# Kernel optimization log

Measured on AMD Instinct MI355X. Metric: run time of the kernel, lower is better.

## Reference

```python
import jax, jax.numpy as jnp
import numpy as np

N = 50000      # nodes
E = 1_600_000  # edges
FN = 8         # num_node_features
FE = 8         # num_edge_features
H = 16         # hidden_layers[0]
IH = 10        # intra_hidden


def _lin(k, i, o):
    return (jax.random.normal(k, (i, o), dtype=jnp.float32) / np.sqrt(i)).astype(jnp.float32)


def setup_inputs() -> dict:
    key = jax.random.key(0)
    ks = jax.random.split(key, 16)
    d = {}
    d["x"] = jax.random.normal(ks[0], (N, FN), dtype=jnp.float32)
    d["edge_attr"] = jax.random.normal(ks[1], (E, FE), dtype=jnp.float32)
    d["edge_index"] = jax.random.randint(ks[2], (2, E), 0, N)
    # NNConv 0: in=FN, out=H; edge-nn: FE -> IH -> FN*H
    d["c0_w1"] = _lin(ks[3], FE, IH);  d["c0_b1"] = jnp.zeros((IH,), jnp.float32)
    d["c0_w2"] = _lin(ks[4], IH, FN * H); d["c0_b2"] = jnp.zeros((FN * H,), jnp.float32)
    d["c0_root"] = _lin(ks[5], FN, H); d["c0_bias"] = jnp.zeros((H,), jnp.float32)
    # NNConv 1: in=H, out=IH; edge-nn: FE -> IH -> H*IH
    d["c1_w1"] = _lin(ks[6], FE, IH);  d["c1_b1"] = jnp.zeros((IH,), jnp.float32)
    d["c1_w2"] = _lin(ks[7], IH, H * IH); d["c1_b2"] = jnp.zeros((H * IH,), jnp.float32)
    d["c1_root"] = _lin(ks[8], H, IH); d["c1_bias"] = jnp.zeros((IH,), jnp.float32)
    # edge predictor: (FE+IH) -> IH -> 1
    d["ep_w1"] = _lin(ks[9], FE + IH, IH); d["ep_b1"] = jnp.zeros((IH,), jnp.float32)
    d["ep_w2"] = _lin(ks[10], IH, 1); d["ep_b2"] = jnp.zeros((1,), jnp.float32)
    return d


def _nnconv(x, edge_index, edge_attr, w1, b1, w2, b2, root, bias, in_ch, out_ch):
    """PyG NNConv (aggr='add', root_weight=True): per-edge weight from edge MLP,
    gather source features, per-edge matvec, scatter-add to targets, plus root term."""
    src, dst = edge_index[0], edge_index[1]
    w = jax.nn.relu(edge_attr @ w1 + b1) @ w2 + b2        # [E, in*out]
    w = w.reshape(-1, in_ch, out_ch)                       # [E, in, out]
    msg = jnp.einsum('ei,eio->eo', x[src], w)              # [E, out]
    agg = jax.ops.segment_sum(msg, dst, num_segments=x.shape[0])  # [N, out]
    return agg + x @ root + bias


def reference(x, edge_attr, edge_index,
              c0_w1, c0_b1, c0_w2, c0_b2, c0_root, c0_bias,
              c1_w1, c1_b1, c1_w2, c1_b2, c1_root, c1_bias,
              ep_w1, ep_b1, ep_w2, ep_b2):
    h = jax.nn.relu(_nnconv(x, edge_index, edge_attr,
                            c0_w1, c0_b1, c0_w2, c0_b2, c0_root, c0_bias, FN, H))
    h = jax.nn.relu(_nnconv(h, edge_index, edge_attr,
                            c1_w1, c1_b1, c1_w2, c1_b2, c1_root, c1_bias, H, IH))
    feat = jnp.concatenate([edge_attr, h[edge_index[0]]], axis=1)  # [E, FE+IH]
    scores = jax.nn.relu(feat @ ep_w1 + ep_b1) @ ep_w2 + ep_b2     # [E, 1]
    return scores.squeeze(-1)
```

## Files before the change

### kernel.cpp

```cpp
#include <hip/hip_runtime.h>

#define N_NODES 50000
#define E_EDGES 1600000
#define FN 8
#define FE 8
#define HID 16
#define IH 10
#define NB_SCAN 196

#define I_CNT   0
#define I_OFF   50048
#define I_RANK  100096
#define I_BSUM  1700096
#define I_BBASE 1700352
#define I_TOTAL 1700608
#define F_H     0
#define F_H2    800000
#define F_MSG   1300000
#define F_TOTAL 26900000
#define WS_NEED ((size_t)I_TOTAL*4 + (size_t)F_TOTAL*4)

__global__ __launch_bounds__(256) void count_rank_k(
    const int* __restrict__ ei, int* __restrict__ cnt, int* __restrict__ rank)
{
    int e = blockIdx.x * 256 + threadIdx.x;
    if (e >= E_EDGES) return;
    int dst = ei[E_EDGES + e];
    rank[e] = atomicAdd(&cnt[dst], 1);
}

__global__ __launch_bounds__(256) void blocksum_k(
    const int* __restrict__ cnt, int* __restrict__ bsum)
{
    __shared__ int sh[256];
    int t = threadIdx.x;
    int idx = blockIdx.x * 256 + t;
    sh[t] = (idx < N_NODES) ? cnt[idx] : 0;
    __syncthreads();
#pragma unroll
    for (int d = 128; d > 0; d >>= 1) {
        if (t < d) sh[t] += sh[t + d];
        __syncthreads();
    }
    if (t == 0) bsum[blockIdx.x] = sh[0];
}

__global__ __launch_bounds__(256) void scan_bsums_k(
    const int* __restrict__ bsum, int* __restrict__ bbase)
{
    __shared__ int sh[256];
    int t = threadIdx.x;
    int v = (t < NB_SCAN) ? bsum[t] : 0;
    sh[t] = v;
    __syncthreads();
#pragma unroll
    for (int d = 1; d < 256; d <<= 1) {
        int u = (t >= d) ? sh[t - d] : 0;
        __syncthreads();
        sh[t] += u;
        __syncthreads();
    }
    if (t < NB_SCAN) bbase[t] = sh[t] - v;
}

__global__ __launch_bounds__(256) void offsets_k(
    const int* __restrict__ cnt, const int* __restrict__ bbase,
    int* __restrict__ offset)
{
    __shared__ int sh[256];
    int t = threadIdx.x;
    int b = blockIdx.x;
    int idx = b * 256 + t;
    int v = (idx < N_NODES) ? cnt[idx] : 0;
    sh[t] = v;
    __syncthreads();
#pragma unroll
    for (int d = 1; d < 256; d <<= 1) {
        int u = (t >= d) ? sh[t - d] : 0;
        __syncthreads();
        sh[t] += u;
        __syncthreads();
    }
    int incl = sh[t];
    int base = bbase[b];
    if (idx < N_NODES) offset[idx] = base + incl - v;
    if (idx == N_NODES - 1) offset[N_NODES] = base + incl;
}

__device__ __forceinline__ void load8(const float* __restrict__ p, float v[8]) {
    const float4* q = reinterpret_cast<const float4*>(p);
    float4 a = q[0], b = q[1];
    v[0]=a.x; v[1]=a.y; v[2]=a.z; v[3]=a.w;
    v[4]=b.x; v[5]=b.y; v[6]=b.z; v[7]=b.w;
}

__device__ __forceinline__ void edge_mlp_seq(
    const float eav[FE], const float* __restrict__ w1,
    const float* __restrict__ b1, float u[IH])
{
#pragma unroll
    for (int h = 0; h < IH; ++h) u[h] = b1[h];
#pragma unroll
    for (int k = 0; k < FE; ++k) {
        float ek = eav[k];
#pragma unroll
        for (int h = 0; h < IH; ++h) u[h] = fmaf(ek, w1[k*IH + h], u[h]);
    }
#pragma unroll
    for (int h = 0; h < IH; ++h) u[h] = fmaxf(u[h], 0.f);
}

__global__ __launch_bounds__(256) void conv0_scatter_k(
    const float* __restrict__ x, const float* __restrict__ ea,
    const int* __restrict__ ei,
    const float* __restrict__ w1, const float* __restrict__ b1,
    const float* __restrict__ w2, const float* __restrict__ b2,
    const int* __restrict__ offset, const int* __restrict__ rank,
    float* __restrict__ msgbuf)
{
    int e = blockIdx.x * 256 + threadIdx.x;
    if (e >= E_EDGES) return;
    int src = ei[e];
    int dst = ei[E_EDGES + e];

    float eav[FE];
    load8(ea + (size_t)e * FE, eav);
    float u[IH];
    edge_mlp_seq(eav, w1, b1, u);
    float xv[FN];
    load8(x + (size_t)src * FN, xv);

    float msg[HID];
#pragma unroll
    for (int o = 0; o < HID; ++o) msg[o] = 0.f;
#pragma unroll
    for (int i = 0; i < FN; ++i) {
        float xi = xv[i];
#pragma unroll
        for (int o = 0; o < HID; ++o)
            msg[o] = fmaf(xi, b2[i*HID + o], msg[o]);
    }
#pragma unroll
    for (int h = 0; h < IH; ++h) {
        float t[HID];
#pragma unroll
        for (int o = 0; o < HID; ++o) t[o] = 0.f;
        const float* wp = w2 + h * (FN*HID);
#pragma unroll
        for (int i = 0; i < FN; ++i) {
            float xi = xv[i];
#pragma unroll
            for (int o = 0; o < HID; ++o)
                t[o] = fmaf(xi, wp[i*HID + o], t[o]);
        }
        float uh = u[h];
#pragma unroll
        for (int o = 0; o < HID; ++o) msg[o] = fmaf(uh, t[o], msg[o]);
    }

    size_t pos = (size_t)(offset[dst] + rank[e]) * HID;
    float4* mp = reinterpret_cast<float4*>(msgbuf + pos);
    mp[0] = make_float4(msg[0],  msg[1],  msg[2],  msg[3]);
    mp[1] = make_float4(msg[4],  msg[5],  msg[6],  msg[7]);
    mp[2] = make_float4(msg[8],  msg[9],  msg[10], msg[11]);
    mp[3] = make_float4(msg[12], msg[13], msg[14], msg[15]);
}

__global__ __launch_bounds__(256) void node0_red_k(
    const float* __restrict__ x, const float* __restrict__ msgbuf,
    const int* __restrict__ offset,
    const float* __restrict__ root, const float* __restrict__ bias,
    float* __restrict__ h)
{
    int idx = blockIdx.x * 256 + threadIdx.x;
    if (idx >= N_NODES * HID) return;
    int n = idx >> 4;
    int o = idx & 15;
    int beg = offset[n], end = offset[n + 1];
    float s = bias[o];
    for (int j = beg; j < end; ++j) s += msgbuf[(size_t)j * HID + o];
    const float* xr = x + (size_t)n * FN;
#pragma unroll
    for (int i = 0; i < FN; ++i) s = fmaf(xr[i], root[i*HID + o], s);
    h[idx] = fmaxf(s, 0.f);
}

__global__ __launch_bounds__(256) void conv1_scatter_k(
    const float* __restrict__ hin, const float* __restrict__ ea,
    const int* __restrict__ ei,
    const float* __restrict__ w1, const float* __restrict__ b1,
    const float* __restrict__ w2, const float* __restrict__ b2,
    const int* __restrict__ offset, const int* __restrict__ rank,
    float* __restrict__ msgbuf)
{
    int e = blockIdx.x * 256 + threadIdx.x;
    if (e >= E_EDGES) return;
    int src = ei[e];
    int dst = ei[E_EDGES + e];

    float eav[FE];
    load8(ea + (size_t)e * FE, eav);
    float u[IH];
    edge_mlp_seq(eav, w1, b1, u);
    float hv[HID];
    load8(hin + (size_t)src * HID,     hv);
    load8(hin + (size_t)src * HID + 8, hv + 8);

    float msg[IH];
#pragma unroll
    for (int o = 0; o < IH; ++o) msg[o] = 0.f;
#pragma unroll
    for (int i = 0; i < HID; ++i) {
        float hi = hv[i];
#pragma unroll
        for (int o = 0; o < IH; ++o)
            msg[o] = fmaf(hi, b2[i*IH + o], msg[o]);
    }
#pragma unroll
    for (int hh = 0; hh < IH; ++hh) {
        float t[IH];
#pragma unroll
        for (int o = 0; o < IH; ++o) t[o] = 0.f;
        const float* wp = w2 + hh * (HID*IH);
#pragma unroll
        for (int i = 0; i < HID; ++i) {
            float hi = hv[i];
#pragma unroll
            for (int o = 0; o < IH; ++o)
                t[o] = fmaf(hi, wp[i*IH + o], t[o]);
        }
        float uh = u[hh];
#pragma unroll
        for (int o = 0; o < IH; ++o) msg[o] = fmaf(uh, t[o], msg[o]);
    }

    size_t pos = (size_t)(offset[dst] + rank[e]) * IH;
    float2* mp = reinterpret_cast<float2*>(msgbuf + pos);
    mp[0] = make_float2(msg[0], msg[1]);
    mp[1] = make_float2(msg[2], msg[3]);
    mp[2] = make_float2(msg[4], msg[5]);
    mp[3] = make_float2(msg[6], msg[7]);
    mp[4] = make_float2(msg[8], msg[9]);
}

__global__ __launch_bounds__(256) void node1_red_k(
    const float* __restrict__ hin, const float* __restrict__ msgbuf,
    const int* __restrict__ offset,
    const float* __restrict__ root, const float* __restrict__ bias,
    float* __restrict__ h2)
{
    int idx = blockIdx.x * 256 + threadIdx.x;
    if (idx >= N_NODES * IH) return;
    int n = idx / IH;
    int o = idx - n * IH;
    int beg = offset[n], end = offset[n + 1];
    float s = bias[o];
    for (int j = beg; j < end; ++j) s += msgbuf[(size_t)j * IH + o];
    const float* hr = hin + (size_t)n * HID;
#pragma unroll
    for (int i = 0; i < HID; ++i) s = fmaf(hr[i], root[i*IH + o], s);
    h2[idx] = fmaxf(s, 0.f);
}

__global__ __launch_bounds__(256) void edge_pred_k(
    const float* __restrict__ h2, const float* __restrict__ ea,
    const int* __restrict__ ei,
    const float* __restrict__ w1, const float* __restrict__ b1,
    const float* __restrict__ w2, const float* __restrict__ b2,
    float* __restrict__ out)
{
    int e = blockIdx.x * 256 + threadIdx.x;
    if (e >= E_EDGES) return;
    int src = ei[e];
    float eav[FE];
    load8(ea + (size_t)e * FE, eav);
    float hv[IH];
    {
        const float2* p = reinterpret_cast<const float2*>(h2 + (size_t)src * IH);
        float2 a = p[0], b = p[1], c = p[2], d = p[3], f = p[4];
        hv[0]=a.x; hv[1]=a.y; hv[2]=b.x; hv[3]=b.y; hv[4]=c.x;
        hv[5]=c.y; hv[6]=d.x; hv[7]=d.y; hv[8]=f.x; hv[9]=f.y;
    }
    float t[IH];
#pragma unroll
    for (int j = 0; j < IH; ++j) t[j] = b1[j];
#pragma unroll
    for (int k = 0; k < FE; ++k) {
        float ek = eav[k];
#pragma unroll
        for (int j = 0; j < IH; ++j) t[j] = fmaf(ek, w1[k*IH + j], t[j]);
    }
#pragma unroll
    for (int k = 0; k < IH; ++k) {
        float hk = hv[k];
#pragma unroll
        for (int j = 0; j < IH; ++j) t[j] = fmaf(hk, w1[(FE + k)*IH + j], t[j]);
    }
    float score = b2[0];
#pragma unroll
    for (int j = 0; j < IH; ++j)
        score = fmaf(fmaxf(t[j], 0.f), w2[j], score);
    out[e] = score;
}

__global__ __launch_bounds__(256) void conv0_edge_k(
    const float* __restrict__ x, const float* __restrict__ ea,
    const int* __restrict__ ei,
    const float* __restrict__ w1, const float* __restrict__ b1,
    const float* __restrict__ w2, const float* __restrict__ b2,
    float* __restrict__ agg)
{
    int e = blockIdx.x * 256 + threadIdx.x;
    if (e >= E_EDGES) return;
    int src = ei[e];
    int dst = ei[E_EDGES + e];
    float eav[FE];
    load8(ea + (size_t)e * FE, eav);
    float u[IH];
    edge_mlp_seq(eav, w1, b1, u);
    float xv[FN];
    load8(x + (size_t)src * FN, xv);
    float msg[HID];
#pragma unroll
    for (int o = 0; o < HID; ++o) msg[o] = 0.f;
#pragma unroll
    for (int i = 0; i < FN; ++i) {
        float xi = xv[i];
#pragma unroll
        for (int o = 0; o < HID; ++o)
            msg[o] = fmaf(xi, b2[i*HID + o], msg[o]);
    }
#pragma unroll
    for (int h = 0; h < IH; ++h) {
        float t[HID];
#pragma unroll
        for (int o = 0; o < HID; ++o) t[o] = 0.f;
        const float* wp = w2 + h * (FN*HID);
#pragma unroll
        for (int i = 0; i < FN; ++i) {
            float xi = xv[i];
#pragma unroll
            for (int o = 0; o < HID; ++o)
                t[o] = fmaf(xi, wp[i*HID + o], t[o]);
        }
        float uh = u[h];
#pragma unroll
        for (int o = 0; o < HID; ++o) msg[o] = fmaf(uh, t[o], msg[o]);
    }
    float* ap = agg + (size_t)dst * HID;
#pragma unroll
    for (int o = 0; o < HID; ++o) atomicAdd(ap + o, msg[o]);
}

__global__ __launch_bounds__(256) void node0_k(
    const float* __restrict__ x, const float* __restrict__ agg,
    const float* __restrict__ root, const float* __restrict__ bias,
    float* __restrict__ h)
{
    int idx = blockIdx.x * 256 + threadIdx.x;
    if (idx >= N_NODES * HID) return;
    int n = idx >> 4;
    int o = idx & 15;
    float s = agg[idx] + bias[o];
    const float* xr = x + (size_t)n * FN;
#pragma unroll
    for (int i = 0; i < FN; ++i) s = fmaf(xr[i], root[i*HID + o], s);
    h[idx] = fmaxf(s, 0.f);
}

__global__ __launch_bounds__(256) void conv1_edge_k(
    const float* __restrict__ hin, const float* __restrict__ ea,
    const int* __restrict__ ei,
    const float* __restrict__ w1, const float* __restrict__ b1,
    const float* __restrict__ w2, const float* __restrict__ b2,
    float* __restrict__ agg)
{
    int e = blockIdx.x * 256 + threadIdx.x;
    if (e >= E_EDGES) return;
    int src = ei[e];
    int dst = ei[E_EDGES + e];
    float eav[FE];
    load8(ea + (size_t)e * FE, eav);
    float u[IH];
    edge_mlp_seq(eav, w1, b1, u);
    float hv[HID];
    load8(hin + (size_t)src * HID,     hv);
    load8(hin + (size_t)src * HID + 8, hv + 8);
    float msg[IH];
#pragma unroll
    for (int o = 0; o < IH; ++o) msg[o] = 0.f;
#pragma unroll
    for (int i = 0; i < HID; ++i) {
        float hi = hv[i];
#pragma unroll
        for (int o = 0; o < IH; ++o)
            msg[o] = fmaf(hi, b2[i*IH + o], msg[o]);
    }
#pragma unroll
    for (int hh = 0; hh < IH; ++hh) {
        float t[IH];
#pragma unroll
        for (int o = 0; o < IH; ++o) t[o] = 0.f;
        const float* wp = w2 + hh * (HID*IH);
#pragma unroll
        for (int i = 0; i < HID; ++i) {
            float hi = hv[i];
#pragma unroll
            for (int o = 0; o < IH; ++o)
                t[o] = fmaf(hi, wp[i*IH + o], t[o]);
        }
        float uh = u[hh];
#pragma unroll
        for (int o = 0; o < IH; ++o) msg[o] = fmaf(uh, t[o], msg[o]);
    }
    float* ap = agg + (size_t)dst * IH;
#pragma unroll
    for (int o = 0; o < IH; ++o) atomicAdd(ap + o, msg[o]);
}

__global__ __launch_bounds__(256) void node1_k(
    const float* __restrict__ hin, const float* __restrict__ agg,
    const float* __restrict__ root, const float* __restrict__ bias,
    float* __restrict__ h2)
{
    int idx = blockIdx.x * 256 + threadIdx.x;
    if (idx >= N_NODES * IH) return;
    int n = idx / IH;
    int o = idx - n * IH;
    float s = agg[idx] + bias[o];
    const float* hr = hin + (size_t)n * HID;
#pragma unroll
    for (int i = 0; i < HID; ++i) s = fmaf(hr[i], root[i*IH + o], s);
    h2[idx] = fmaxf(s, 0.f);
}

extern "C" void kernel_launch(void* const* d_in, const int* in_sizes, int n_in,
                              void* d_out, int out_size, void* d_ws, size_t ws_size,
                              hipStream_t stream) {
    const float* x       = (const float*)d_in[0];
    const float* ea      = (const float*)d_in[1];
    const int*   ei      = (const int*)  d_in[2];
    const float* c0_w1   = (const float*)d_in[3];
    const float* c0_b1   = (const float*)d_in[4];
    const float* c0_w2   = (const float*)d_in[5];
    const float* c0_b2   = (const float*)d_in[6];
    const float* c0_root = (const float*)d_in[7];
    const float* c0_bias = (const float*)d_in[8];
    const float* c1_w1   = (const float*)d_in[9];
    const float* c1_b1   = (const float*)d_in[10];
    const float* c1_w2   = (const float*)d_in[11];
    const float* c1_b2   = (const float*)d_in[12];
    const float* c1_root = (const float*)d_in[13];
    const float* c1_bias = (const float*)d_in[14];
    const float* ep_w1   = (const float*)d_in[15];
    const float* ep_b1   = (const float*)d_in[16];
    const float* ep_w2   = (const float*)d_in[17];
    const float* ep_b2   = (const float*)d_in[18];
    float* out = (float*)d_out;

    int eb = (E_EDGES + 255) / 256;

    if (ws_size >= WS_NEED) {
        int*   wi     = (int*)d_ws;
        int*   cnt    = wi + I_CNT;
        int*   offset = wi + I_OFF;
        int*   rank   = wi + I_RANK;
        int*   bsum   = wi + I_BSUM;
        int*   bbase  = wi + I_BBASE;
        float* wf     = (float*)(wi + I_TOTAL);
        float* h      = wf + F_H;
        float* h2     = wf + F_H2;
        float* msg    = wf + F_MSG;

        hipMemsetAsync(cnt, 0, N_NODES * sizeof(int), stream);
        count_rank_k<<<eb, 256, 0, stream>>>(ei, cnt, rank);
        blocksum_k<<<NB_SCAN, 256, 0, stream>>>(cnt, bsum);
        scan_bsums_k<<<1, 256, 0, stream>>>(bsum, bbase);
        offsets_k<<<NB_SCAN, 256, 0, stream>>>(cnt, bbase, offset);

        conv0_scatter_k<<<eb, 256, 0, stream>>>(x, ea, ei, c0_w1, c0_b1, c0_w2, c0_b2,
                                                offset, rank, msg);
        node0_red_k<<<(N_NODES*HID + 255)/256, 256, 0, stream>>>(x, msg, offset,
                                                                 c0_root, c0_bias, h);
        conv1_scatter_k<<<eb, 256, 0, stream>>>(h, ea, ei, c1_w1, c1_b1, c1_w2, c1_b2,
                                                offset, rank, msg);
        node1_red_k<<<(N_NODES*IH + 255)/256, 256, 0, stream>>>(h, msg, offset,
                                                                c1_root, c1_bias, h2);
        edge_pred_k<<<eb, 256, 0, stream>>>(h2, ea, ei, ep_w1, ep_b1, ep_w2, ep_b2, out);
    } else {
        float* ws   = (float*)d_ws;
        float* agg0 = ws;
        float* agg1 = ws + 800000;
        float* h    = ws + 1300000;
        float* h2   = ws + 2100000;
        hipMemsetAsync(d_ws, 0, 1300000 * sizeof(float), stream);
        conv0_edge_k<<<eb, 256, 0, stream>>>(x, ea, ei, c0_w1, c0_b1, c0_w2, c0_b2, agg0);
        node0_k<<<(N_NODES*HID + 255)/256, 256, 0, stream>>>(x, agg0, c0_root, c0_bias, h);
        conv1_edge_k<<<eb, 256, 0, stream>>>(h, ea, ei, c1_w1, c1_b1, c1_w2, c1_b2, agg1);
        node1_k<<<(N_NODES*IH + 255)/256, 256, 0, stream>>>(h, agg1, c1_root, c1_bias, h2);
        edge_pred_k<<<eb, 256, 0, stream>>>(h2, ea, ei, ep_w1, ep_b1, ep_w2, ep_b2, out);
    }
}
```

Baseline: 300.1 us.

## Write edge messages in edge order and gather via CSR permutation in reduction

Instead of scattering each edge message to its destination-sorted slot using rank, the conv kernels now write messages contiguously by edge index. A separate cursor and perm pass builds a destination-sorted edge permutation, and the node reduction kernels read messages indirectly through it. This trades scattered writes in the edge kernels for coalesced writes, at the cost of an extra atomic pass and indirect gathered reads in the reductions.

Measured after the change: 476.4 us. 1.59x slower.

```diff
diff --git a/kernel.cpp b/kernel.cpp
--- a/kernel.cpp
+++ b/kernel.cpp
@@ -10,7 +10,7 @@
 
 #define I_CNT   0
 #define I_OFF   50048
-#define I_RANK  100096
+#define I_PERM  100096
 #define I_BSUM  1700096
 #define I_BBASE 1700352
 #define I_TOTAL 1700608
@@ -20,13 +20,12 @@
 #define F_TOTAL 26900000
 #define WS_NEED ((size_t)I_TOTAL*4 + (size_t)F_TOTAL*4)
 
-__global__ __launch_bounds__(256) void count_rank_k(
-    const int* __restrict__ ei, int* __restrict__ cnt, int* __restrict__ rank)
-{
-    int e = blockIdx.x * 256 + threadIdx.x;
-    if (e >= E_EDGES) return;
-    int dst = ei[E_EDGES + e];
-    rank[e] = atomicAdd(&cnt[dst], 1);
+__global__ __launch_bounds__(256) void count_k(
+    const int* __restrict__ ei, int* __restrict__ cnt)
+{
+    int e = blockIdx.x * 256 + threadIdx.x;
+    if (e >= E_EDGES) return;
+    atomicAdd(&cnt[ei[E_EDGES + e]], 1);
 }
 
 __global__ __launch_bounds__(256) void blocksum_k(
@@ -87,6 +86,22 @@
     if (idx == N_NODES - 1) offset[N_NODES] = base + incl;
 }
 
+__global__ __launch_bounds__(256) void cursor_k(
+    const int* __restrict__ offset, int* __restrict__ cursor)
+{
+    int n = blockIdx.x * 256 + threadIdx.x;
+    if (n < N_NODES) cursor[n] = offset[n];
+}
+
+__global__ __launch_bounds__(256) void perm_k(
+    const int* __restrict__ ei, int* __restrict__ cursor, int* __restrict__ perm)
+{
+    int e = blockIdx.x * 256 + threadIdx.x;
+    if (e >= E_EDGES) return;
+    int pos = atomicAdd(&cursor[ei[E_EDGES + e]], 1);
+    perm[pos] = e;
+}
+
 __device__ __forceinline__ void load8(const float* __restrict__ p, float v[8]) {
     const float4* q = reinterpret_cast<const float4*>(p);
     float4 a = q[0], b = q[1];
@@ -110,18 +125,16 @@
     for (int h = 0; h < IH; ++h) u[h] = fmaxf(u[h], 0.f);
 }
 
-__global__ __launch_bounds__(256) void conv0_scatter_k(
+__global__ __launch_bounds__(256) void conv0_seq_k(
     const float* __restrict__ x, const float* __restrict__ ea,
     const int* __restrict__ ei,
     const float* __restrict__ w1, const float* __restrict__ b1,
     const float* __restrict__ w2, const float* __restrict__ b2,
-    const int* __restrict__ offset, const int* __restrict__ rank,
     float* __restrict__ msgbuf)
 {
     int e = blockIdx.x * 256 + threadIdx.x;
     if (e >= E_EDGES) return;
     int src = ei[e];
-    int dst = ei[E_EDGES + e];
 
     float eav[FE];
     load8(ea + (size_t)e * FE, eav);
@@ -158,17 +171,16 @@
         for (int o = 0; o < HID; ++o) msg[o] = fmaf(uh, t[o], msg[o]);
     }
 
-    size_t pos = (size_t)(offset[dst] + rank[e]) * HID;
-    float4* mp = reinterpret_cast<float4*>(msgbuf + pos);
+    float4* mp = reinterpret_cast<float4*>(msgbuf + (size_t)e * HID);
     mp[0] = make_float4(msg[0],  msg[1],  msg[2],  msg[3]);
     mp[1] = make_float4(msg[4],  msg[5],  msg[6],  msg[7]);
     mp[2] = make_float4(msg[8],  msg[9],  msg[10], msg[11]);
     mp[3] = make_float4(msg[12], msg[13], msg[14], msg[15]);
 }
 
-__global__ __launch_bounds__(256) void node0_red_k(
+__global__ __launch_bounds__(256) void node0_perm_k(
     const float* __restrict__ x, const float* __restrict__ msgbuf,
-    const int* __restrict__ offset,
+    const int* __restrict__ offset, const int* __restrict__ perm,
     const float* __restrict__ root, const float* __restrict__ bias,
     float* __restrict__ h)
 {
@@ -178,25 +190,26 @@
     int o = idx & 15;
     int beg = offset[n], end = offset[n + 1];
     float s = bias[o];
-    for (int j = beg; j < end; ++j) s += msgbuf[(size_t)j * HID + o];
+    for (int j = beg; j < end; ++j) {
+        int e2 = perm[j];
+        s += msgbuf[(size_t)e2 * HID + o];
+    }
     const float* xr = x + (size_t)n * FN;
 #pragma unroll
     for (int i = 0; i < FN; ++i) s = fmaf(xr[i], root[i*HID + o], s);
     h[idx] = fmaxf(s, 0.f);
 }
 
-__global__ __launch_bounds__(256) void conv1_scatter_k(
+__global__ __launch_bounds__(256) void conv1_seq_k(
     const float* __restrict__ hin, const float* __restrict__ ea,
     const int* __restrict__ ei,
     const float* __restrict__ w1, const float* __restrict__ b1,
     const float* __restrict__ w2, const float* __restrict__ b2,
-    const int* __restrict__ offset, const int* __restrict__ rank,
     float* __restrict__ msgbuf)
 {
     int e = blockIdx.x * 256 + threadIdx.x;
     if (e >= E_EDGES) return;
     int src = ei[e];
-    int dst = ei[E_EDGES + e];
 
     float eav[FE];
     load8(ea + (size_t)e * FE, eav);
@@ -234,8 +247,7 @@
         for (int o = 0; o < IH; ++o) msg[o] = fmaf(uh, t[o], msg[o]);
     }
 
-    size_t pos = (size_t)(offset[dst] + rank[e]) * IH;
-    float2* mp = reinterpret_cast<float2*>(msgbuf + pos);
+    float2* mp = reinterpret_cast<float2*>(msgbuf + (size_t)e * IH);
     mp[0] = make_float2(msg[0], msg[1]);
     mp[1] = make_float2(msg[2], msg[3]);
     mp[2] = make_float2(msg[4], msg[5]);
@@ -243,9 +255,9 @@
     mp[4] = make_float2(msg[8], msg[9]);
 }
 
-__global__ __launch_bounds__(256) void node1_red_k(
+__global__ __launch_bounds__(256) void node1_perm_k(
     const float* __restrict__ hin, const float* __restrict__ msgbuf,
-    const int* __restrict__ offset,
+    const int* __restrict__ offset, const int* __restrict__ perm,
     const float* __restrict__ root, const float* __restrict__ bias,
     float* __restrict__ h2)
 {
@@ -255,7 +267,10 @@
     int o = idx - n * IH;
     int beg = offset[n], end = offset[n + 1];
     float s = bias[o];
-    for (int j = beg; j < end; ++j) s += msgbuf[(size_t)j * IH + o];
+    for (int j = beg; j < end; ++j) {
+        int e2 = perm[j];
+        s += msgbuf[(size_t)e2 * IH + o];
+    }
     const float* hr = hin + (size_t)n * HID;
 #pragma unroll
     for (int i = 0; i < HID; ++i) s = fmaf(hr[i], root[i*IH + o], s);
@@ -464,7 +479,7 @@
         int*   wi     = (int*)d_ws;
         int*   cnt    = wi + I_CNT;
         int*   offset = wi + I_OFF;
-        int*   rank   = wi + I_RANK;
+        int*   perm   = wi + I_PERM;
         int*   bsum   = wi + I_BSUM;
         int*   bbase  = wi + I_BBASE;
         float* wf     = (float*)(wi + I_TOTAL);
@@ -473,19 +488,19 @@
         float* msg    = wf + F_MSG;
 
         hipMemsetAsync(cnt, 0, N_NODES * sizeof(int), stream);
-        count_rank_k<<<eb, 256, 0, stream>>>(ei, cnt, rank);
+        count_k<<<eb, 256, 0, stream>>>(ei, cnt);
         blocksum_k<<<NB_SCAN, 256, 0, stream>>>(cnt, bsum);
         scan_bsums_k<<<1, 256, 0, stream>>>(bsum, bbase);
         offsets_k<<<NB_SCAN, 256, 0, stream>>>(cnt, bbase, offset);
-
-        conv0_scatter_k<<<eb, 256, 0, stream>>>(x, ea, ei, c0_w1, c0_b1, c0_w2, c0_b2,
-                                                offset, rank, msg);
-        node0_red_k<<<(N_NODES*HID + 255)/256, 256, 0, stream>>>(x, msg, offset,
-                                                                 c0_root, c0_bias, h);
-        conv1_scatter_k<<<eb, 256, 0, stream>>>(h, ea, ei, c1_w1, c1_b1, c1_w2, c1_b2,
-                                                offset, rank, msg);
-        node1_red_k<<<(N_NODES*IH + 255)/256, 256, 0, stream>>>(h, msg, offset,
-                                                                c1_root, c1_bias, h2);
+        cursor_k<<<NB_SCAN, 256, 0, stream>>>(offset, cnt);
+        perm_k<<<eb, 256, 0, stream>>>(ei, cnt, perm);
+
+        conv0_seq_k<<<eb, 256, 0, stream>>>(x, ea, ei, c0_w1, c0_b1, c0_w2, c0_b2, msg);
+        node0_perm_k<<<(N_NODES*HID + 255)/256, 256, 0, stream>>>(x, msg, offset, perm,
+                                                                  c0_root, c0_bias, h);
+        conv1_seq_k<<<eb, 256, 0, stream>>>(h, ea, ei, c1_w1, c1_b1, c1_w2, c1_b2, msg);
+        node1_perm_k<<<(N_NODES*IH + 255)/256, 256, 0, stream>>>(h, msg, offset, perm,
+                                                                 c1_root, c1_bias, h2);
         edge_pred_k<<<eb, 256, 0, stream>>>(h2, ea, ei, ep_w1, ep_b1, ep_w2, ep_b2, out);
     } else {
         float* ws   = (float*)d_ws;
```

## Store edge messages in bf16 and pad atomic counters to separate cache lines

Applied to the files above, without the earlier changes.

Per-edge messages written by the scatter kernels and read by the node reductions are now packed as bf16 (16 or 12 shorts per edge), which halves or more the scratch-buffer traffic. The per-node degree counters are spread 64 bytes apart, with the counter array placed in the message region, so that atomics on different nodes avoid sharing a cache line. Rounding messages to bf16 adds precision loss to the aggregated sums. The padded counter memset is larger, and the counter scan now reads with a strided pattern.

New measurement: 598.0 us. 1.99x slower.

```diff
diff --git a/kernel.cpp b/kernel.cpp
--- a/kernel.cpp
+++ b/kernel.cpp
@@ -1,4 +1,5 @@
 #include <hip/hip_runtime.h>
+#include <hip/hip_bf16.h>
 
 #define N_NODES 50000
 #define E_EDGES 1600000
@@ -8,7 +9,6 @@
 #define IH 10
 #define NB_SCAN 196
 
-#define I_CNT   0
 #define I_OFF   50048
 #define I_RANK  100096
 #define I_BSUM  1700096
@@ -21,21 +21,21 @@
 #define WS_NEED ((size_t)I_TOTAL*4 + (size_t)F_TOTAL*4)
 
 __global__ __launch_bounds__(256) void count_rank_k(
-    const int* __restrict__ ei, int* __restrict__ cnt, int* __restrict__ rank)
+    const int* __restrict__ ei, int* __restrict__ cntP, int* __restrict__ rank)
 {
     int e = blockIdx.x * 256 + threadIdx.x;
     if (e >= E_EDGES) return;
     int dst = ei[E_EDGES + e];
-    rank[e] = atomicAdd(&cnt[dst], 1);
+    rank[e] = atomicAdd(&cntP[dst * 16], 1);
 }
 
 __global__ __launch_bounds__(256) void blocksum_k(
-    const int* __restrict__ cnt, int* __restrict__ bsum)
+    const int* __restrict__ cntP, int* __restrict__ bsum)
 {
     __shared__ int sh[256];
     int t = threadIdx.x;
     int idx = blockIdx.x * 256 + t;
-    sh[t] = (idx < N_NODES) ? cnt[idx] : 0;
+    sh[t] = (idx < N_NODES) ? cntP[idx * 16] : 0;
     __syncthreads();
 #pragma unroll
     for (int d = 128; d > 0; d >>= 1) {
@@ -64,14 +64,14 @@
 }
 
 __global__ __launch_bounds__(256) void offsets_k(
-    const int* __restrict__ cnt, const int* __restrict__ bbase,
+    const int* __restrict__ cntP, const int* __restrict__ bbase,
     int* __restrict__ offset)
 {
     __shared__ int sh[256];
     int t = threadIdx.x;
     int b = blockIdx.x;
     int idx = b * 256 + t;
-    int v = (idx < N_NODES) ? cnt[idx] : 0;
+    int v = (idx < N_NODES) ? cntP[idx * 16] : 0;
     sh[t] = v;
     __syncthreads();
 #pragma unroll
@@ -108,6 +108,16 @@
     }
 #pragma unroll
     for (int h = 0; h < IH; ++h) u[h] = fmaxf(u[h], 0.f);
+}
+
+__device__ __forceinline__ unsigned pkbf(float a, float b) {
+    union { __hip_bfloat162 v; unsigned u; } r;
+    r.v = __hip_bfloat162(__float2bfloat16(a), __float2bfloat16(b));
+    return r.u;
+}
+
+__device__ __forceinline__ float upbf(unsigned short us) {
+    return __uint_as_float(((unsigned)us) << 16);
 }
 
 __global__ __launch_bounds__(256) void conv0_scatter_k(
@@ -116,7 +126,7 @@
     const float* __restrict__ w1, const float* __restrict__ b1,
     const float* __restrict__ w2, const float* __restrict__ b2,
     const int* __restrict__ offset, const int* __restrict__ rank,
-    float* __restrict__ msgbuf)
+    unsigned short* __restrict__ msg16)
 {
     int e = blockIdx.x * 256 + threadIdx.x;
     if (e >= E_EDGES) return;
@@ -158,16 +168,19 @@
         for (int o = 0; o < HID; ++o) msg[o] = fmaf(uh, t[o], msg[o]);
     }
 
-    size_t pos = (size_t)(offset[dst] + rank[e]) * HID;
-    float4* mp = reinterpret_cast<float4*>(msgbuf + pos);
-    mp[0] = make_float4(msg[0],  msg[1],  msg[2],  msg[3]);
-    mp[1] = make_float4(msg[4],  msg[5],  msg[6],  msg[7]);
-    mp[2] = make_float4(msg[8],  msg[9],  msg[10], msg[11]);
-    mp[3] = make_float4(msg[12], msg[13], msg[14], msg[15]);
+    size_t pos = (size_t)(offset[dst] + rank[e]);
+    unsigned short* mp = msg16 + pos * 16;
+    uint4 a0, a1;
+    a0.x = pkbf(msg[0],  msg[1]);  a0.y = pkbf(msg[2],  msg[3]);
+    a0.z = pkbf(msg[4],  msg[5]);  a0.w = pkbf(msg[6],  msg[7]);
+    a1.x = pkbf(msg[8],  msg[9]);  a1.y = pkbf(msg[10], msg[11]);
+    a1.z = pkbf(msg[12], msg[13]); a1.w = pkbf(msg[14], msg[15]);
+    *reinterpret_cast<uint4*>(mp)     = a0;
+    *reinterpret_cast<uint4*>(mp + 8) = a1;
 }
 
 __global__ __launch_bounds__(256) void node0_red_k(
-    const float* __restrict__ x, const float* __restrict__ msgbuf,
+    const float* __restrict__ x, const unsigned short* __restrict__ msg16,
     const int* __restrict__ offset,
     const float* __restrict__ root, const float* __restrict__ bias,
     float* __restrict__ h)
@@ -178,7 +191,7 @@
     int o = idx & 15;
     int beg = offset[n], end = offset[n + 1];
     float s = bias[o];
-    for (int j = beg; j < end; ++j) s += msgbuf[(size_t)j * HID + o];
+    for (int j = beg; j < end; ++j) s += upbf(msg16[(size_t)j * 16 + o]);
     const float* xr = x + (size_t)n * FN;
 #pragma unroll
     for (int i = 0; i < FN; ++i) s = fmaf(xr[i], root[i*HID + o], s);
@@ -191,7 +204,7 @@
     const float* __restrict__ w1, const float* __restrict__ b1,
     const float* __restrict__ w2, const float* __restrict__ b2,
     const int* __restrict__ offset, const int* __restrict__ rank,
-    float* __restrict__ msgbuf)
+    unsigned short* __restrict__ msg16)
 {
     int e = blockIdx.x * 256 + threadIdx.x;
     if (e >= E_EDGES) return;
@@ -234,17 +247,19 @@
         for (int o = 0; o < IH; ++o) msg[o] = fmaf(uh, t[o], msg[o]);
     }
 
-    size_t pos = (size_t)(offset[dst] + rank[e]) * IH;
-    float2* mp = reinterpret_cast<float2*>(msgbuf + pos);
-    mp[0] = make_float2(msg[0], msg[1]);
-    mp[1] = make_float2(msg[2], msg[3]);
-    mp[2] = make_float2(msg[4], msg[5]);
-    mp[3] = make_float2(msg[6], msg[7]);
-    mp[4] = make_float2(msg[8], msg[9]);
+    size_t pos = (size_t)(offset[dst] + rank[e]);
+    unsigned short* mp = msg16 + pos * 12;
+    uint2 b0, b1v, b2v;
+    b0.x  = pkbf(msg[0], msg[1]);  b0.y  = pkbf(msg[2], msg[3]);
+    b1v.x = pkbf(msg[4], msg[5]);  b1v.y = pkbf(msg[6], msg[7]);
+    b2v.x = pkbf(msg[8], msg[9]);  b2v.y = 0u;
+    *reinterpret_cast<uint2*>(mp)     = b0;
+    *reinterpret_cast<uint2*>(mp + 4) = b1v;
+    *reinterpret_cast<uint2*>(mp + 8) = b2v;
 }
 
 __global__ __launch_bounds__(256) void node1_red_k(
-    const float* __restrict__ hin, const float* __restrict__ msgbuf,
+    const float* __restrict__ hin, const unsigned short* __restrict__ msg16,
     const int* __restrict__ offset,
     const float* __restrict__ root, const float* __restrict__ bias,
     float* __restrict__ h2)
@@ -255,7 +270,7 @@
     int o = idx - n * IH;
     int beg = offset[n], end = offset[n + 1];
     float s = bias[o];
-    for (int j = beg; j < end; ++j) s += msgbuf[(size_t)j * IH + o];
+    for (int j = beg; j < end; ++j) s += upbf(msg16[(size_t)j * 12 + o]);
     const float* hr = hin + (size_t)n * HID;
 #pragma unroll
     for (int i = 0; i < HID; ++i) s = fmaf(hr[i], root[i*IH + o], s);
@@ -462,7 +477,6 @@
 
     if (ws_size >= WS_NEED) {
         int*   wi     = (int*)d_ws;
-        int*   cnt    = wi + I_CNT;
         int*   offset = wi + I_OFF;
         int*   rank   = wi + I_RANK;
         int*   bsum   = wi + I_BSUM;
@@ -470,21 +484,22 @@
         float* wf     = (float*)(wi + I_TOTAL);
         float* h      = wf + F_H;
         float* h2     = wf + F_H2;
-        float* msg    = wf + F_MSG;
-
-        hipMemsetAsync(cnt, 0, N_NODES * sizeof(int), stream);
-        count_rank_k<<<eb, 256, 0, stream>>>(ei, cnt, rank);
-        blocksum_k<<<NB_SCAN, 256, 0, stream>>>(cnt, bsum);
+        int*            cntP  = (int*)(wf + F_MSG);
+        unsigned short* msg16 = (unsigned short*)(wf + F_MSG);
+
+        hipMemsetAsync(cntP, 0, (size_t)N_NODES * 16 * sizeof(int), stream);
+        count_rank_k<<<eb, 256, 0, stream>>>(ei, cntP, rank);
+        blocksum_k<<<NB_SCAN, 256, 0, stream>>>(cntP, bsum);
         scan_bsums_k<<<1, 256, 0, stream>>>(bsum, bbase);
-        offsets_k<<<NB_SCAN, 256, 0, stream>>>(cnt, bbase, offset);
+        offsets_k<<<NB_SCAN, 256, 0, stream>>>(cntP, bbase, offset);
 
         conv0_scatter_k<<<eb, 256, 0, stream>>>(x, ea, ei, c0_w1, c0_b1, c0_w2, c0_b2,
-                                                offset, rank, msg);
-        node0_red_k<<<(N_NODES*HID + 255)/256, 256, 0, stream>>>(x, msg, offset,
+                                                offset, rank, msg16);
+        node0_red_k<<<(N_NODES*HID + 255)/256, 256, 0, stream>>>(x, msg16, offset,
                                                                  c0_root, c0_bias, h);
         conv1_scatter_k<<<eb, 256, 0, stream>>>(h, ea, ei, c1_w1, c1_b1, c1_w2, c1_b2,
-                                                offset, rank, msg);
-        node1_red_k<<<(N_NODES*IH + 255)/256, 256, 0, stream>>>(h, msg, offset,
+                                                offset, rank, msg16);
+        node1_red_k<<<(N_NODES*IH + 255)/256, 256, 0, stream>>>(h, msg16, offset,
                                                                 c1_root, c1_bias, h2);
         edge_pred_k<<<eb, 256, 0, stream>>>(h2, ea, ei, ep_w1, ep_b1, ep_w2, ep_b2, out);
     } else {
```

## Pad atomic counters to 64B and stage scatter writes through LDS as float4

Applied to the files above, without the earlier changes.

Counters for the per-destination atomic count are padded to one per 64-byte slot, placed in the message buffer region, so atomics on different nodes do not share cache lines. The conv scatter kernels stage each edge's message in shared memory and then write it cooperatively, four threads per edge, as float4 stores, making each row write a full 64-byte segment. Conv1 messages are padded from 10 to 16 floats to allow this. The trade-offs are a larger memset, more bytes written and read for conv1, an extra block barrier, and removal of the edge bounds check, which is safe only because E is a multiple of 256.

Measured after the change: 283.5 us. 5.5% less time.

```diff
diff --git a/kernel.cpp b/kernel.cpp
--- a/kernel.cpp
+++ b/kernel.cpp
@@ -8,7 +8,6 @@
 #define IH 10
 #define NB_SCAN 196
 
-#define I_CNT   0
 #define I_OFF   50048
 #define I_RANK  100096
 #define I_BSUM  1700096
@@ -21,21 +20,21 @@
 #define WS_NEED ((size_t)I_TOTAL*4 + (size_t)F_TOTAL*4)
 
 __global__ __launch_bounds__(256) void count_rank_k(
-    const int* __restrict__ ei, int* __restrict__ cnt, int* __restrict__ rank)
+    const int* __restrict__ ei, int* __restrict__ cntP, int* __restrict__ rank)
 {
     int e = blockIdx.x * 256 + threadIdx.x;
     if (e >= E_EDGES) return;
     int dst = ei[E_EDGES + e];
-    rank[e] = atomicAdd(&cnt[dst], 1);
+    rank[e] = atomicAdd(&cntP[dst * 16], 1);
 }
 
 __global__ __launch_bounds__(256) void blocksum_k(
-    const int* __restrict__ cnt, int* __restrict__ bsum)
+    const int* __restrict__ cntP, int* __restrict__ bsum)
 {
     __shared__ int sh[256];
     int t = threadIdx.x;
     int idx = blockIdx.x * 256 + t;
-    sh[t] = (idx < N_NODES) ? cnt[idx] : 0;
+    sh[t] = (idx < N_NODES) ? cntP[idx * 16] : 0;
     __syncthreads();
 #pragma unroll
     for (int d = 128; d > 0; d >>= 1) {
@@ -64,14 +63,14 @@
 }
 
 __global__ __launch_bounds__(256) void offsets_k(
-    const int* __restrict__ cnt, const int* __restrict__ bbase,
+    const int* __restrict__ cntP, const int* __restrict__ bbase,
     int* __restrict__ offset)
 {
     __shared__ int sh[256];
     int t = threadIdx.x;
     int b = blockIdx.x;
     int idx = b * 256 + t;
-    int v = (idx < N_NODES) ? cnt[idx] : 0;
+    int v = (idx < N_NODES) ? cntP[idx * 16] : 0;
     sh[t] = v;
     __syncthreads();
 #pragma unroll
@@ -118,10 +117,14 @@
     const int* __restrict__ offset, const int* __restrict__ rank,
     float* __restrict__ msgbuf)
 {
-    int e = blockIdx.x * 256 + threadIdx.x;
-    if (e >= E_EDGES) return;
+    __shared__ float smsg[256 * 17];
+    __shared__ int   plds[256];
+
+    int t = threadIdx.x;
+    int e = blockIdx.x * 256 + t;
     int src = ei[e];
     int dst = ei[E_EDGES + e];
+    plds[t] = offset[dst] + rank[e];
 
     float eav[FE];
     load8(ea + (size_t)e * FE, eav);
@@ -142,28 +145,35 @@
     }
 #pragma unroll
     for (int h = 0; h < IH; ++h) {
-        float t[HID];
-#pragma unroll
-        for (int o = 0; o < HID; ++o) t[o] = 0.f;
+        float tt[HID];
+#pragma unroll
+        for (int o = 0; o < HID; ++o) tt[o] = 0.f;
         const float* wp = w2 + h * (FN*HID);
 #pragma unroll
         for (int i = 0; i < FN; ++i) {
             float xi = xv[i];
 #pragma unroll
             for (int o = 0; o < HID; ++o)
-                t[o] = fmaf(xi, wp[i*HID + o], t[o]);
+                tt[o] = fmaf(xi, wp[i*HID + o], tt[o]);
         }
         float uh = u[h];
 #pragma unroll
-        for (int o = 0; o < HID; ++o) msg[o] = fmaf(uh, t[o], msg[o]);
-    }
-
-    size_t pos = (size_t)(offset[dst] + rank[e]) * HID;
-    float4* mp = reinterpret_cast<float4*>(msgbuf + pos);
-    mp[0] = make_float4(msg[0],  msg[1],  msg[2],  msg[3]);
-    mp[1] = make_float4(msg[4],  msg[5],  msg[6],  msg[7]);
-    mp[2] = make_float4(msg[8],  msg[9],  msg[10], msg[11]);
-    mp[3] = make_float4(msg[12], msg[13], msg[14], msg[15]);
+        for (int o = 0; o < HID; ++o) msg[o] = fmaf(uh, tt[o], msg[o]);
+    }
+
+#pragma unroll
+    for (int o = 0; o < HID; ++o) smsg[t*17 + o] = msg[o];
+    __syncthreads();
+
+    int q   = t & 3;
+    int eb0 = t >> 2;
+#pragma unroll
+    for (int rep = 0; rep < 4; ++rep) {
+        int eL  = eb0 + rep * 64;
+        int pos = plds[eL];
+        float4 v = *reinterpret_cast<const float4*>(&smsg[eL*17 + q*4]);
+        *reinterpret_cast<float4*>(msgbuf + (size_t)pos * 16 + q * 4) = v;
+    }
 }
 
 __global__ __launch_bounds__(256) void node0_red_k(
@@ -178,7 +188,7 @@
     int o = idx & 15;
     int beg = offset[n], end = offset[n + 1];
     float s = bias[o];
-    for (int j = beg; j < end; ++j) s += msgbuf[(size_t)j * HID + o];
+    for (int j = beg; j < end; ++j) s += msgbuf[(size_t)j * 16 + o];
     const float* xr = x + (size_t)n * FN;
 #pragma unroll
     for (int i = 0; i < FN; ++i) s = fmaf(xr[i], root[i*HID + o], s);
@@ -193,10 +203,14 @@
     const int* __restrict__ offset, const int* __restrict__ rank,
     float* __restrict__ msgbuf)
 {
-    int e = blockIdx.x * 256 + threadIdx.x;
-    if (e >= E_EDGES) return;
+    __shared__ float smsg[256 * 17];
+    __shared__ int   plds[256];
+
+    int t = threadIdx.x;
+    int e = blockIdx.x * 256 + t;
     int src = ei[e];
     int dst = ei[E_EDGES + e];
+    plds[t] = offset[dst] + rank[e];
 
     float eav[FE];
     load8(ea + (size_t)e * FE, eav);
@@ -206,9 +220,9 @@
     load8(hin + (size_t)src * HID,     hv);
     load8(hin + (size_t)src * HID + 8, hv + 8);
 
-    float msg[IH];
-#pragma unroll
-    for (int o = 0; o < IH; ++o) msg[o] = 0.f;
+    float msg[HID];
+#pragma unroll
+    for (int o = 0; o < HID; ++o) msg[o] = 0.f;
 #pragma unroll
     for (int i = 0; i < HID; ++i) {
         float hi = hv[i];
@@ -218,29 +232,35 @@
     }
 #pragma unroll
     for (int hh = 0; hh < IH; ++hh) {
-        float t[IH];
-#pragma unroll
-        for (int o = 0; o < IH; ++o) t[o] = 0.f;
+        float tt[IH];
+#pragma unroll
+        for (int o = 0; o < IH; ++o) tt[o] = 0.f;
         const float* wp = w2 + hh * (HID*IH);
 #pragma unroll
         for (int i = 0; i < HID; ++i) {
             float hi = hv[i];
 #pragma unroll
             for (int o = 0; o < IH; ++o)
-                t[o] = fmaf(hi, wp[i*IH + o], t[o]);
+                tt[o] = fmaf(hi, wp[i*IH + o], tt[o]);
         }
         float uh = u[hh];
 #pragma unroll
-        for (int o = 0; o < IH; ++o) msg[o] = fmaf(uh, t[o], msg[o]);
-    }
-
-    size_t pos = (size_t)(offset[dst] + rank[e]) * IH;
-    float2* mp = reinterpret_cast<float2*>(msgbuf + pos);
-    mp[0] = make_float2(msg[0], msg[1]);
-    mp[1] = make_float2(msg[2], msg[3]);
-    mp[2] = make_float2(msg[4], msg[5]);
-    mp[3] = make_float2(msg[6], msg[7]);
-    mp[4] = make_float2(msg[8], msg[9]);
+        for (int o = 0; o < IH; ++o) msg[o] = fmaf(uh, tt[o], msg[o]);
+    }
+
+#pragma unroll
+    for (int o = 0; o < HID; ++o) smsg[t*17 + o] = msg[o];
+    __syncthreads();
+
+    int q   = t & 3;
+    int eb0 = t >> 2;
+#pragma unroll
+    for (int rep = 0; rep < 4; ++rep) {
+        int eL  = eb0 + rep * 64;
+        int pos = plds[eL];
+        float4 v = *reinterpret_cast<const float4*>(&smsg[eL*17 + q*4]);
+        *reinterpret_cast<float4*>(msgbuf + (size_t)pos * 16 + q * 4) = v;
+    }
 }
 
 __global__ __launch_bounds__(256) void node1_red_k(
@@ -255,7 +275,7 @@
     int o = idx - n * IH;
     int beg = offset[n], end = offset[n + 1];
     float s = bias[o];
-    for (int j = beg; j < end; ++j) s += msgbuf[(size_t)j * IH + o];
+    for (int j = beg; j < end; ++j) s += msgbuf[(size_t)j * 16 + o];
     const float* hr = hin + (size_t)n * HID;
 #pragma unroll
     for (int i = 0; i < HID; ++i) s = fmaf(hr[i], root[i*IH + o], s);
@@ -462,7 +482,6 @@
 
     if (ws_size >= WS_NEED) {
         int*   wi     = (int*)d_ws;
-        int*   cnt    = wi + I_CNT;
         int*   offset = wi + I_OFF;
         int*   rank   = wi + I_RANK;
         int*   bsum   = wi + I_BSUM;
@@ -471,12 +490,13 @@
         float* h      = wf + F_H;
         float* h2     = wf + F_H2;
         float* msg    = wf + F_MSG;
-
-        hipMemsetAsync(cnt, 0, N_NODES * sizeof(int), stream);
-        count_rank_k<<<eb, 256, 0, stream>>>(ei, cnt, rank);
-        blocksum_k<<<NB_SCAN, 256, 0, stream>>>(cnt, bsum);
+        int*   cntP   = (int*)(wf + F_MSG);
+
+        hipMemsetAsync(cntP, 0, (size_t)N_NODES * 16 * sizeof(int), stream);
+        count_rank_k<<<eb, 256, 0, stream>>>(ei, cntP, rank);
+        blocksum_k<<<NB_SCAN, 256, 0, stream>>>(cntP, bsum);
         scan_bsums_k<<<1, 256, 0, stream>>>(bsum, bbase);
-        offsets_k<<<NB_SCAN, 256, 0, stream>>>(cnt, bbase, offset);
+        offsets_k<<<NB_SCAN, 256, 0, stream>>>(cntP, bbase, offset);
 
         conv0_scatter_k<<<eb, 256, 0, stream>>>(x, ea, ei, c0_w1, c0_b1, c0_w2, c0_b2,
                                                 offset, rank, msg);
```
